# Kernel tuning notes

Measured on AMD Instinct MI355X. Metric: run time of the kernel, lower is better.

## Reference

```python
import jax, jax.numpy as jnp
import numpy as np
import math

B, C, H, W = 32, 384, 64, 64      # batch, backbone dim, feature-map HxW
E, NH = 256, 16                   # embed_dim, num_heads (grapsules per image)
HD = E // NH                      # head dim
RFF_HALF, HID = 32, 128           # RFF rows (out=64), GNN hidden


def setup_inputs() -> dict:
    key = jax.random.key(0)
    ks = jax.random.split(key, 10)
    rn = lambda k, s: (0.02 * jax.random.normal(k, s)).astype(jnp.float32)
    x = jax.random.normal(ks[0], (B, C, H, W), jnp.float32)
    qw = rn(ks[1], (E, C)); qb = jnp.zeros((E,), jnp.float32)
    kw = rn(ks[2], (E, C)); kb = jnp.zeros((E,), jnp.float32)
    vw = rn(ks[3], (E, C)); vb = jnp.zeros((E,), jnp.float32)
    # RFF B ~ N(0,1) * sigma * 2*pi, sigma=1.0
    B_rff = (jax.random.normal(ks[4], (RFF_HALF, 2)) * (2.0 * math.pi)).astype(jnp.float32)
    msg_w = rn(ks[5], (HID, E)); msg_b = jnp.zeros((HID,), jnp.float32)
    emb_w = rn(ks[6], (HID, 2 * RFF_HALF))
    lin1_w = rn(ks[7], (4 * HID, HID)); lin1_b = jnp.zeros((4 * HID,), jnp.float32)
    lin2_w = rn(ks[8], (E, 4 * HID)); lin2_b = jnp.zeros((E,), jnp.float32)
    layer_scale = jnp.full((1, E), 1e-6, jnp.float32)
    # fully-connected directed graph (no self loops) among the NH grapsules of each image
    pairs = np.array([(i, j) for i in range(NH) for j in range(NH) if i != j], dtype=np.int32)
    off = (np.arange(B, dtype=np.int32) * NH)[:, None]
    edge_src = jnp.asarray((pairs[:, 0][None, :] + off).reshape(-1))
    edge_dst = jnp.asarray((pairs[:, 1][None, :] + off).reshape(-1))
    return dict(x=x, qw=qw, qb=qb, kw=kw, kb=kb, vw=vw, vb=vb, B_rff=B_rff,
                msg_w=msg_w, msg_b=msg_b, emb_w=emb_w, lin1_w=lin1_w, lin1_b=lin1_b,
                lin2_w=lin2_w, lin2_b=lin2_b, layer_scale=layer_scale,
                edge_src=edge_src, edge_dst=edge_dst)


def _forward(x, qw, qb, kw, kb, vw, vb, B_rff, msg_w, msg_b, emb_w,
             lin1_w, lin1_b, lin2_w, lin2_b, layer_scale, edge_src, edge_dst):
    Bsz, Cc, Hh, Ww = x.shape
    N = Hh * Ww
    # --- ImageToGraphTransformer (attention pooling to grapsule nodes) ---
    xf = x.reshape(Bsz, Cc, N).transpose(0, 2, 1)            # [B,N,C]
    xm = xf.mean(axis=1)                                     # [B,C]
    q = (xm @ qw.T + qb).reshape(Bsz, NH, HD)                # [B,h,d]
    k = (xf @ kw.T + kb).reshape(Bsz, N, NH, HD)             # [B,N,h,d]
    v = xf @ vw.T + vb                                       # [B,N,E]
    logits = jnp.einsum('bhc,bnhc->bnh', q, k) / math.sqrt(HD)
    attn = jax.nn.softmax(logits, axis=1)                    # softmax over pixels
    xx, yy = jnp.meshgrid(jnp.arange(Hh, dtype=x.dtype), jnp.arange(Ww, dtype=x.dtype), indexing='ij')
    pos_grid = jnp.stack((xx.reshape(-1), yy.reshape(-1)), axis=-1)  # [N,2]
    values = jnp.einsum('bnh,bnc->bhc', attn, v).reshape(Bsz * NH, E)
    pos = jnp.einsum('bnh,nx->bhx', attn, pos_grid).reshape(Bsz * NH, 2)
    # --- RFF embedding of relative positions (edge_attr) ---
    rel = pos[edge_src] - pos[edge_dst]                      # [Eg,2]
    proj = rel @ B_rff.T                                     # [Eg,32]
    edge_attr = math.sqrt(2.0) * jnp.concatenate((jnp.sin(proj), jnp.cos(proj)), axis=-1)
    # --- Conv (MessagePassing) with ConditionalLinear 'strong', mean aggr ---
    m = (values[edge_src] @ msg_w.T + msg_b) * (edge_attr @ emb_w.T)   # [Eg,HID]
    agg = jax.ops.segment_sum(m, edge_dst, num_segments=Bsz * NH) / (NH - 1)
    # --- ConvBlockNeXt MLP + layer scale + identity skip (in==out) ---
    h = jax.nn.silu(agg @ lin1_w.T + lin1_b)
    o = h @ lin2_w.T + lin2_b
    return layer_scale * o + values


def reference(x, qw, qb, kw, kb, vw, vb, B_rff, msg_w, msg_b, emb_w,
              lin1_w, lin1_b, lin2_w, lin2_b, layer_scale, edge_src, edge_dst):
    return _forward(x, qw, qb, kw, kb, vw, vb, B_rff, msg_w, msg_b, emb_w,
                    lin1_w, lin1_b, lin2_w, lin2_b, layer_scale, edge_src, edge_dst)
```

## Files before the change

kernel.cpp:

```cpp
#include <hip/hip_runtime.h>
#include <math.h>


#define Bsz 32
#define Cc  384
#define Nn  4096
#define Ee  256
#define NHh 16
#define HIDh 128

__device__ __forceinline__ float waveSum(float v){
#pragma unroll
  for(int o=32;o;o>>=1) v += __shfl_down(v,(unsigned)o,64);
  return v;
}
__device__ __forceinline__ float waveSumAll(float v){
#pragma unroll
  for(int o=1;o<64;o<<=1) v += __shfl_xor(v,(unsigned)o,64);
  return v;
}
__device__ __forceinline__ float blockSum(float v, float* sm){
  int lane = threadIdx.x & 63, w = threadIdx.x >> 6;
  int nw = blockDim.x >> 6;
  float r = waveSum(v);
  if(lane==0) sm[w] = r;
  __syncthreads();
  float s = 0.f;
  for(int i=0;i<nw;i++) s += sm[i];
  __syncthreads();
  return s;
}

__global__ __launch_bounds__(256) void k_mean(const float* __restrict__ x, float* __restrict__ xm){
  int bc = blockIdx.x, t = threadIdx.x;
  const float4* xr = (const float4*)(x + (size_t)bc*Nn);
  float s = 0.f;
#pragma unroll
  for(int i=0;i<4;i++){ float4 v = xr[t + 256*i]; s += (v.x+v.y) + (v.z+v.w); }
  __shared__ float sm[8];
  s = blockSum(s, sm);
  if(t==0) xm[bc] = s * (1.0f/4096.0f);
}

__global__ __launch_bounds__(384) void k_qk(const float* __restrict__ xm, const float* __restrict__ qw,
                                            const float* __restrict__ qb, const float* __restrict__ kw,
                                            float* __restrict__ qk_t){
  int b = blockIdx.x, t = threadIdx.x;
  __shared__ float xs[Cc];
  __shared__ float qs[Ee];
  if(t < 96) ((float4*)xs)[t] = ((const float4*)(xm + b*Cc))[t];
  __syncthreads();
  if(t < Ee){
    const float4* wr = (const float4*)(qw + (size_t)t*Cc);
    const float4* xv = (const float4*)xs;
    float a = qb[t];
#pragma unroll 4
    for(int c4=0;c4<96;c4++){ float4 w = wr[c4], xx = xv[c4]; a += w.x*xx.x + w.y*xx.y + w.z*xx.z + w.w*xx.w; }
    qs[t] = a;
  }
  __syncthreads();
  int c = t;
#pragma unroll
  for(int hq=0; hq<4; hq++){
    float r0, r1, r2, r3;
#pragma unroll
    for(int hh=0; hh<4; hh++){
      int h = hq*4 + hh;
      float a = 0.f;
#pragma unroll
      for(int d=0; d<16; d++) a += qs[h*16+d] * kw[(size_t)(h*16+d)*Cc + c];
      a *= 0.25f;
      if(hh==0) r0=a; else if(hh==1) r1=a; else if(hh==2) r2=a; else r3=a;
    }
    ((float4*)(qk_t + ((size_t)b*Cc + c)*16))[hq] = make_float4(r0,r1,r2,r3);
  }
}

#define XLS 20
#define ELS 260
__global__ __launch_bounds__(256, 3) void k_attn(const float* __restrict__ x, const float* __restrict__ qk_t,
                                                 float* __restrict__ spart, float* __restrict__ part){
  __shared__ float u0[Cc*XLS];
  __shared__ float el[16*ELS];
  float* qks = u0;
  float* xl  = u0;
  int b = blockIdx.y, ns = blockIdx.x, t = threadIdx.x;
  int n = ns*256 + t;

  {
    const float4* src = (const float4*)(qk_t + (size_t)b*Cc*16);
    float4* dst = (float4*)qks;
#pragma unroll
    for(int i=0;i<6;i++) dst[t + 256*i] = src[t + 256*i];
  }
  __syncthreads();

  float acc[16];
#pragma unroll
  for(int h=0;h<16;h++) acc[h] = 0.f;
  {
    const float* xb = x + (size_t)b*Cc*Nn + n;
#pragma unroll 8
    for(int c=0;c<Cc;c++){
      float xv = xb[(size_t)c*Nn];
      const float4* qv = (const float4*)(qks + c*16);
      float4 q0 = qv[0], q1 = qv[1], q2 = qv[2], q3 = qv[3];
      acc[0]  += xv*q0.x; acc[1]  += xv*q0.y; acc[2]  += xv*q0.z; acc[3]  += xv*q0.w;
      acc[4]  += xv*q1.x; acc[5]  += xv*q1.y; acc[6]  += xv*q1.z; acc[7]  += xv*q1.w;
      acc[8]  += xv*q2.x; acc[9]  += xv*q2.y; acc[10] += xv*q2.z; acc[11] += xv*q2.w;
      acc[12] += xv*q3.x; acc[13] += xv*q3.y; acc[14] += xv*q3.z; acc[15] += xv*q3.w;
    }
  }

#pragma unroll
  for(int h=0;h<16;h++) el[h*ELS + t] = __expf(acc[h]);

  int th = t & 3, tc = t >> 2;
  float4 xr[6];
  auto LOAD = [&](int ch){
    int n0 = ns*256 + ch*16;
#pragma unroll
    for(int i=0;i<6;i++){
      int f = t + 256*i;
      int c = f >> 2, j4 = f & 3;
      xr[i] = *(const float4*)(x + ((size_t)(b*Cc+c))*Nn + n0 + j4*4);
    }
  };
  LOAD(0);
  __syncthreads();

  {
    int w = t >> 6, lane = t & 63;
#pragma unroll
    for(int hh=0; hh<4; hh++){
      int h = w*4 + hh;
      float e0 = el[h*ELS + lane],       e1 = el[h*ELS + 64 + lane];
      float e2 = el[h*ELS + 128 + lane], e3 = el[h*ELS + 192 + lane];
      float row0 = (float)(ns*4);
      float col  = (float)lane;
      float s  = (e0+e1)+(e2+e3);
      float px = e0*row0 + e1*(row0+1.f) + e2*(row0+2.f) + e3*(row0+3.f);
      float py = s * col;
      float s_t  = waveSumAll(s);
      float px_t = waveSumAll(px);
      float py_t = waveSumAll(py);
      if(lane==0)
        *(float4*)(spart + ((size_t)(b*16+h)*16 + ns)*4) = make_float4(s_t, px_t, py_t, 0.f);
    }
  }

  float acc2[4][6];
#pragma unroll
  for(int k=0;k<4;k++)
#pragma unroll
    for(int m=0;m<6;m++) acc2[k][m] = 0.f;

  for(int ch=0; ch<16; ch++){
#pragma unroll
    for(int i=0;i<6;i++){
      int f = t + 256*i;
      int c = f >> 2, j4 = f & 3;
      *(float4*)(xl + c*XLS + j4*4) = xr[i];
    }
    __syncthreads();
    if(ch < 15) LOAD(ch+1);
    int n0l = ch*16;
#pragma unroll
    for(int j4=0;j4<4;j4++){
      float4 a4[4], x4[6];
#pragma unroll
      for(int k=0;k<4;k++) a4[k] = *(const float4*)(el + (th+4*k)*ELS + n0l + j4*4);
#pragma unroll
      for(int m=0;m<6;m++) x4[m] = *(const float4*)(xl + (tc+64*m)*XLS + j4*4);
#pragma unroll
      for(int k=0;k<4;k++)
#pragma unroll
        for(int m=0;m<6;m++)
          acc2[k][m] += a4[k].x*x4[m].x + a4[k].y*x4[m].y + a4[k].z*x4[m].z + a4[k].w*x4[m].w;
    }
    __syncthreads();
  }
#pragma unroll
  for(int k=0;k<4;k++)
#pragma unroll
    for(int m=0;m<6;m++)
      part[(size_t)ns*(Bsz*NHh*Cc) + (size_t)(b*16 + th + 4*k)*Cc + (tc + 64*m)] = acc2[k][m];
}

__global__ __launch_bounds__(256) void k_values(const float* __restrict__ part, const float* __restrict__ spart,
                                                const float* __restrict__ vw, const float* __restrict__ vb,
                                                const float* __restrict__ msg_w, const float* __restrict__ msg_b,
                                                float* __restrict__ values, float* __restrict__ msgv,
                                                float* __restrict__ pos){
  int node = blockIdx.x, t = threadIdx.x;
  __shared__ float xa[Cc];
  __shared__ float vs[Ee];
  __shared__ float invs;
  if(t < 16){
    float4 sp = ((const float4*)spart)[node*16 + t];
    float s = sp.x, px = sp.y, py = sp.z;
    s  += __shfl_xor(s,1u,64);  s  += __shfl_xor(s,2u,64);
    s  += __shfl_xor(s,4u,64);  s  += __shfl_xor(s,8u,64);
    px += __shfl_xor(px,1u,64); px += __shfl_xor(px,2u,64);
    px += __shfl_xor(px,4u,64); px += __shfl_xor(px,8u,64);
    py += __shfl_xor(py,1u,64); py += __shfl_xor(py,2u,64);
    py += __shfl_xor(py,4u,64); py += __shfl_xor(py,8u,64);
    if(t==0){
      float iv = 1.0f/s;
      invs = iv;
      pos[node*2] = px*iv; pos[node*2+1] = py*iv;
    }
  }
  __syncthreads();
  if(t < 96){
    float iv = invs;
    float4 s = make_float4(0,0,0,0);
#pragma unroll
    for(int p=0;p<16;p++){
      float4 v = *(const float4*)(part + (size_t)p*(Bsz*NHh*Cc) + (size_t)node*Cc + t*4);
      s.x += v.x; s.y += v.y; s.z += v.z; s.w += v.w;
    }
    *(float4*)(xa + t*4) = make_float4(s.x*iv, s.y*iv, s.z*iv, s.w*iv);
  }
  __syncthreads();
  {
    const float4* wr = (const float4*)(vw + (size_t)t*Cc);
    const float4* xv = (const float4*)xa;
    float a = vb[t];
#pragma unroll 4
    for(int c4=0;c4<96;c4++){ float4 w = wr[c4], xx = xv[c4]; a += w.x*xx.x + w.y*xx.y + w.z*xx.z + w.w*xx.w; }
    values[(size_t)node*Ee + t] = a;
    vs[t] = a;
  }
  __syncthreads();
  if(t < HIDh){
    const float4* mr = (const float4*)(msg_w + (size_t)t*Ee);
    const float4* vv = (const float4*)vs;
    float a = msg_b[t];
#pragma unroll 4
    for(int e4=0;e4<64;e4++){ float4 w = mr[e4], xx = vv[e4]; a += w.x*xx.x + w.y*xx.y + w.z*xx.z + w.w*xx.w; }
    msgv[(size_t)node*HIDh + t] = a;
  }
}

__global__ __launch_bounds__(256) void k_aggmlp(const float* __restrict__ pos, const float* __restrict__ msgv,
        const float* __restrict__ brff, const float* __restrict__ emb_w,
        const float* __restrict__ l1w, const float* __restrict__ l1b,
        const float* __restrict__ l2w, const float* __restrict__ l2b,
        const float* __restrict__ ls, const float* __restrict__ values, float* __restrict__ out){
  int node = blockIdx.x, t = threadIdx.x;
  int b = node >> 4, jj = node & 15;
  __shared__ float ps[32];
  __shared__ float bf[64];
  __shared__ float mv[16*HIDh];
  __shared__ float ea[64];
  __shared__ float ag[HIDh];
  __shared__ float h1[512];
  if(t < 32) ps[t] = pos[b*32 + t];
  if(t < 64) bf[t] = brff[t];
#pragma unroll
  for(int i=0;i<2;i++){ int f = t + 256*i; ((float4*)mv)[f] = ((const float4*)(msgv + (size_t)b*16*HIDh))[f]; }
  float4 er[16];
  if(t < HIDh){
#pragma unroll
    for(int k=0;k<16;k++) er[k] = ((const float4*)(emb_w + (size_t)t*64))[k];
  }
  __syncthreads();
  float pxj = ps[jj*2], pyj = ps[jj*2+1];
  float acc = 0.f;
  for(int i=0;i<16;i++){
    if(i == jj) continue;
    float rx = ps[i*2]   - pxj;
    float ry = ps[i*2+1] - pyj;
    __syncthreads();
    if(t < 32){
      float pr = rx*bf[t*2] + ry*bf[t*2+1];
      ea[t]    = 1.41421356f * __sinf(pr);
      ea[t+32] = 1.41421356f * __cosf(pr);
    }
    __syncthreads();
    if(t < HIDh){
      float psi = 0.f;
      const float4* eav = (const float4*)ea;
#pragma unroll
      for(int k=0;k<16;k++){ float4 e4 = eav[k]; psi += e4.x*er[k].x + e4.y*er[k].y + e4.z*er[k].z + e4.w*er[k].w; }
      acc += mv[i*HIDh + t] * psi;
    }
  }
  if(t < HIDh) ag[t] = acc * (1.0f/15.0f);
  __syncthreads();
#pragma unroll
  for(int r=0;r<2;r++){
    int u = t + r*256;
    const float4* wr = (const float4*)(l1w + (size_t)u*HIDh);
    const float4* av = (const float4*)ag;
    float a = l1b[u];
#pragma unroll 4
    for(int k=0;k<32;k++){ float4 w = wr[k], xx = av[k]; a += w.x*xx.x + w.y*xx.y + w.z*xx.z + w.w*xx.w; }
    h1[u] = a / (1.0f + __expf(-a));
  }
  __syncthreads();
  {
    const float4* wr = (const float4*)(l2w + (size_t)t*512);
    const float4* hv = (const float4*)h1;
    float o = l2b[t];
#pragma unroll 4
    for(int k=0;k<128;k++){ float4 w = wr[k], xx = hv[k]; o += w.x*xx.x + w.y*xx.y + w.z*xx.z + w.w*xx.w; }
    size_t oi = (size_t)node*Ee + t;
    out[oi] = ls[t]*o + values[oi];
  }
}

extern "C" void kernel_launch(void* const* d_in, const int* in_sizes, int n_in,
                              void* d_out, int out_size, void* d_ws, size_t ws_size,
                              hipStream_t stream) {
  const float* x    = (const float*)d_in[0];
  const float* qw   = (const float*)d_in[1];
  const float* qb   = (const float*)d_in[2];
  const float* kw   = (const float*)d_in[3];
  const float* vw   = (const float*)d_in[5];
  const float* vb   = (const float*)d_in[6];
  const float* brff = (const float*)d_in[7];
  const float* msgw = (const float*)d_in[8];
  const float* msgb = (const float*)d_in[9];
  const float* embw = (const float*)d_in[10];
  const float* l1w  = (const float*)d_in[11];
  const float* l1b  = (const float*)d_in[12];
  const float* l2w  = (const float*)d_in[13];
  const float* l2b  = (const float*)d_in[14];
  const float* lsc  = (const float*)d_in[15];

  float* W      = (float*)d_ws;
  float* xm     = W;
  float* qkt    = xm  + 12288;
  float* spart  = qkt + 196608;
  float* part   = spart + 32768;
  float* values = part + 3145728;
  float* msgv   = values + 131072;
  float* pos    = msgv + 65536;
  float* out    = (float*)d_out;

  k_mean  <<<Bsz*Cc, 256, 0, stream>>>(x, xm);
  k_qk    <<<Bsz, 384, 0, stream>>>(xm, qw, qb, kw, qkt);
  k_attn  <<<dim3(16, Bsz), 256, 0, stream>>>(x, qkt, spart, part);
  k_values<<<Bsz*NHh, 256, 0, stream>>>(part, spart, vw, vb, msgw, msgb, values, msgv, pos);
  k_aggmlp<<<Bsz*NHh, 256, 0, stream>>>(pos, msgv, brff, embw, l1w, l1b, l2w, l2b, lsc, values, out);
}
```

Measured before the change: 593.6 us.

## Double spatial tile per attention block to halve partial sums

Each k_attn block now covers 512 spatial positions instead of 256. Each thread computes two positions' logits with float2 loads, and chunks of 32 columns are staged through LDS. Launching 8 blocks per image instead of 16 halves the partial-sum buffer that k_values must reduce and halves the redundant q·k staging. The cost is much larger LDS use per block (about 88 KB versus 47 KB), more registers from 32 accumulators and 12 prefetch float4s, and only 256 blocks in total, so occupancy and parallelism drop.

```diff
diff --git a/kernel.cpp b/kernel.cpp
--- a/kernel.cpp
+++ b/kernel.cpp
@@ -76,16 +76,16 @@
   }
 }
 
-#define XLS 20
-#define ELS 260
-__global__ __launch_bounds__(256, 3) void k_attn(const float* __restrict__ x, const float* __restrict__ qk_t,
-                                                 float* __restrict__ spart, float* __restrict__ part){
-  __shared__ float u0[Cc*XLS];
+#define XROW 36
+#define ELS  516
+__global__ __launch_bounds__(256) void k_attn(const float* __restrict__ x, const float* __restrict__ qk_t,
+                                              float* __restrict__ spart, float* __restrict__ part){
+  __shared__ float u0[Cc*XROW];
   __shared__ float el[16*ELS];
   float* qks = u0;
   float* xl  = u0;
   int b = blockIdx.y, ns = blockIdx.x, t = threadIdx.x;
-  int n = ns*256 + t;
+  int n0 = ns*512 + 2*t;
 
   {
     const float4* src = (const float4*)(qk_t + (size_t)b*Cc*16);
@@ -95,35 +95,48 @@
   }
   __syncthreads();
 
-  float acc[16];
-#pragma unroll
-  for(int h=0;h<16;h++) acc[h] = 0.f;
-  {
-    const float* xb = x + (size_t)b*Cc*Nn + n;
+  float ax[16], ay[16];
+#pragma unroll
+  for(int h=0;h<16;h++){ ax[h]=0.f; ay[h]=0.f; }
+  {
+    const float* xb = x + (size_t)b*Cc*Nn + n0;
 #pragma unroll 8
     for(int c=0;c<Cc;c++){
-      float xv = xb[(size_t)c*Nn];
+      float2 xv = *(const float2*)(xb + (size_t)c*Nn);
       const float4* qv = (const float4*)(qks + c*16);
       float4 q0 = qv[0], q1 = qv[1], q2 = qv[2], q3 = qv[3];
-      acc[0]  += xv*q0.x; acc[1]  += xv*q0.y; acc[2]  += xv*q0.z; acc[3]  += xv*q0.w;
-      acc[4]  += xv*q1.x; acc[5]  += xv*q1.y; acc[6]  += xv*q1.z; acc[7]  += xv*q1.w;
-      acc[8]  += xv*q2.x; acc[9]  += xv*q2.y; acc[10] += xv*q2.z; acc[11] += xv*q2.w;
-      acc[12] += xv*q3.x; acc[13] += xv*q3.y; acc[14] += xv*q3.z; acc[15] += xv*q3.w;
-    }
-  }
-
-#pragma unroll
-  for(int h=0;h<16;h++) el[h*ELS + t] = __expf(acc[h]);
+      ax[0]  += xv.x*q0.x; ay[0]  += xv.y*q0.x;
+      ax[1]  += xv.x*q0.y; ay[1]  += xv.y*q0.y;
+      ax[2]  += xv.x*q0.z; ay[2]  += xv.y*q0.z;
+      ax[3]  += xv.x*q0.w; ay[3]  += xv.y*q0.w;
+      ax[4]  += xv.x*q1.x; ay[4]  += xv.y*q1.x;
+      ax[5]  += xv.x*q1.y; ay[5]  += xv.y*q1.y;
+      ax[6]  += xv.x*q1.z; ay[6]  += xv.y*q1.z;
+      ax[7]  += xv.x*q1.w; ay[7]  += xv.y*q1.w;
+      ax[8]  += xv.x*q2.x; ay[8]  += xv.y*q2.x;
+      ax[9]  += xv.x*q2.y; ay[9]  += xv.y*q2.y;
+      ax[10] += xv.x*q2.z; ay[10] += xv.y*q2.z;
+      ax[11] += xv.x*q2.w; ay[11] += xv.y*q2.w;
+      ax[12] += xv.x*q3.x; ay[12] += xv.y*q3.x;
+      ax[13] += xv.x*q3.y; ay[13] += xv.y*q3.y;
+      ax[14] += xv.x*q3.z; ay[14] += xv.y*q3.z;
+      ax[15] += xv.x*q3.w; ay[15] += xv.y*q3.w;
+    }
+  }
+
+#pragma unroll
+  for(int h=0;h<16;h++)
+    *(float2*)(el + h*ELS + 2*t) = make_float2(__expf(ax[h]), __expf(ay[h]));
 
   int th = t & 3, tc = t >> 2;
-  float4 xr[6];
+  float4 xr[12];
   auto LOAD = [&](int ch){
-    int n0 = ns*256 + ch*16;
-#pragma unroll
-    for(int i=0;i<6;i++){
+    int nb = ns*512 + ch*32;
+#pragma unroll
+    for(int i=0;i<12;i++){
       int f = t + 256*i;
-      int c = f >> 2, j4 = f & 3;
-      xr[i] = *(const float4*)(x + ((size_t)(b*Cc+c))*Nn + n0 + j4*4);
+      int c = f >> 3, j4 = f & 7;
+      xr[i] = *(const float4*)(x + ((size_t)(b*Cc+c))*Nn + nb + j4*4);
     }
   };
   LOAD(0);
@@ -134,18 +147,26 @@
 #pragma unroll
     for(int hh=0; hh<4; hh++){
       int h = w*4 + hh;
-      float e0 = el[h*ELS + lane],       e1 = el[h*ELS + 64 + lane];
-      float e2 = el[h*ELS + 128 + lane], e3 = el[h*ELS + 192 + lane];
-      float row0 = (float)(ns*4);
-      float col  = (float)lane;
-      float s  = (e0+e1)+(e2+e3);
-      float px = e0*row0 + e1*(row0+1.f) + e2*(row0+2.f) + e3*(row0+3.f);
-      float py = s * col;
+      float s = 0.f, px = 0.f, py = 0.f;
+#pragma unroll
+      for(int half=0; half<2; half++){
+        float4 e4 = *(const float4*)(el + h*ELS + half*256 + 4*lane);
+#pragma unroll
+        for(int j=0;j<4;j++){
+          float e = (j==0)?e4.x:((j==1)?e4.y:((j==2)?e4.z:e4.w));
+          int nl = ns*512 + half*256 + 4*lane + j;
+          s  += e;
+          px += e * (float)(nl >> 6);
+          py += e * (float)(nl & 63);
+        }
+      }
       float s_t  = waveSumAll(s);
       float px_t = waveSumAll(px);
       float py_t = waveSumAll(py);
-      if(lane==0)
-        *(float4*)(spart + ((size_t)(b*16+h)*16 + ns)*4) = make_float4(s_t, px_t, py_t, 0.f);
+      if(lane==0){
+        float4* sp = (float4*)(spart + ((size_t)(b*16+h)*8 + ns)*4);
+        *sp = make_float4(s_t, px_t, py_t, 0.f);
+      }
     }
   }
 
@@ -157,21 +178,21 @@
 
   for(int ch=0; ch<16; ch++){
 #pragma unroll
-    for(int i=0;i<6;i++){
+    for(int i=0;i<12;i++){
       int f = t + 256*i;
-      int c = f >> 2, j4 = f & 3;
-      *(float4*)(xl + c*XLS + j4*4) = xr[i];
+      int c = f >> 3, j4 = f & 7;
+      *(float4*)(xl + c*XROW + j4*4) = xr[i];
     }
     __syncthreads();
     if(ch < 15) LOAD(ch+1);
-    int n0l = ch*16;
-#pragma unroll
-    for(int j4=0;j4<4;j4++){
+    int n0l = ch*32;
+#pragma unroll
+    for(int j4=0;j4<8;j4++){
       float4 a4[4], x4[6];
 #pragma unroll
       for(int k=0;k<4;k++) a4[k] = *(const float4*)(el + (th+4*k)*ELS + n0l + j4*4);
 #pragma unroll
-      for(int m=0;m<6;m++) x4[m] = *(const float4*)(xl + (tc+64*m)*XLS + j4*4);
+      for(int m=0;m<6;m++) x4[m] = *(const float4*)(xl + (tc+64*m)*XROW + j4*4);
 #pragma unroll
       for(int k=0;k<4;k++)
 #pragma unroll
@@ -196,15 +217,12 @@
   __shared__ float xa[Cc];
   __shared__ float vs[Ee];
   __shared__ float invs;
-  if(t < 16){
-    float4 sp = ((const float4*)spart)[node*16 + t];
+  if(t < 8){
+    float4 sp = ((const float4*)spart)[node*8 + t];
     float s = sp.x, px = sp.y, py = sp.z;
-    s  += __shfl_xor(s,1u,64);  s  += __shfl_xor(s,2u,64);
-    s  += __shfl_xor(s,4u,64);  s  += __shfl_xor(s,8u,64);
-    px += __shfl_xor(px,1u,64); px += __shfl_xor(px,2u,64);
-    px += __shfl_xor(px,4u,64); px += __shfl_xor(px,8u,64);
-    py += __shfl_xor(py,1u,64); py += __shfl_xor(py,2u,64);
-    py += __shfl_xor(py,4u,64); py += __shfl_xor(py,8u,64);
+    s  += __shfl_xor(s,1u,64);  s  += __shfl_xor(s,2u,64);  s  += __shfl_xor(s,4u,64);
+    px += __shfl_xor(px,1u,64); px += __shfl_xor(px,2u,64); px += __shfl_xor(px,4u,64);
+    py += __shfl_xor(py,1u,64); py += __shfl_xor(py,2u,64); py += __shfl_xor(py,4u,64);
     if(t==0){
       float iv = 1.0f/s;
       invs = iv;
@@ -216,7 +234,7 @@
     float iv = invs;
     float4 s = make_float4(0,0,0,0);
 #pragma unroll
-    for(int p=0;p<16;p++){
+    for(int p=0;p<8;p++){
       float4 v = *(const float4*)(part + (size_t)p*(Bsz*NHh*Cc) + (size_t)node*Cc + t*4);
       s.x += v.x; s.y += v.y; s.z += v.z; s.w += v.w;
     }
@@ -334,15 +352,15 @@
   float* xm     = W;
   float* qkt    = xm  + 12288;
   float* spart  = qkt + 196608;
-  float* part   = spart + 32768;
-  float* values = part + 3145728;
+  float* part   = spart + 16384;
+  float* values = part + 1572864;
   float* msgv   = values + 131072;
   float* pos    = msgv + 65536;
   float* out    = (float*)d_out;
 
   k_mean  <<<Bsz*Cc, 256, 0, stream>>>(x, xm);
   k_qk    <<<Bsz, 384, 0, stream>>>(xm, qw, qb, kw, qkt);
-  k_attn  <<<dim3(16, Bsz), 256, 0, stream>>>(x, qkt, spart, part);
+  k_attn  <<<dim3(8, Bsz), 256, 0, stream>>>(x, qkt, spart, part);
   k_values<<<Bsz*NHh, 256, 0, stream>>>(part, spart, vw, vb, msgw, msgb, values, msgv, pos);
   k_aggmlp<<<Bsz*NHh, 256, 0, stream>>>(pos, msgv, brff, embw, l1w, l1b, l2w, l2b, lsc, values, out);
 }
```

After: 521.4 us. -12.2%, faster.
